# Optimization experiments

Measured on AMD Instinct MI355X. Metric: run time of the kernel, lower is better.

The kernel has to match this reference:

```python
import jax, jax.numpy as jnp
import numpy as np
import math

HIDDEN = 1024
NUM_HEADS = 16
NUM_GROUPS = 16  # source einsum/rearrange only shape-checks when groups == heads
HEAD_DIM = HIDDEN // NUM_HEADS


def rope(x, base=10000.0):
    # x: [b, s, d]; applied to the FULL hidden vector before head split, as in source.
    # Source rope_fn has a reshape bug; this is the intended rotate-half RoPE with
    # half_d frequencies 1/base^(i/half_d) (== 1/base^(2i/d)).
    b, s, d = x.shape
    half = d // 2
    x1, x2 = x[..., :half], x[..., half:]
    pos = jnp.arange(s, dtype=x.dtype)[:, None]                          # [s,1]
    inv_freq = 1.0 / (base ** (jnp.arange(half, dtype=x.dtype) / half))  # [half]
    ang = pos * inv_freq[None, :]                                        # [s,half]
    sin = jnp.sin(ang)[None]                                             # [1,s,half]
    cos = jnp.cos(ang)[None]
    return jnp.concatenate([x1 * cos - x2 * sin, x2 * cos + x1 * sin], axis=-1)


def setup_inputs() -> dict:
    key = jax.random.key(0)
    ks = jax.random.split(key, 10)
    scale = 1.0 / math.sqrt(HIDDEN)
    inp = {
        "x": jax.random.normal(ks[0], (2, 2048, HIDDEN), dtype=jnp.float32),
        "attn_mask": jax.random.randint(ks[1], (2, 2048), 0, 2, dtype=jnp.int32),
        "Wq": jax.random.uniform(ks[2], (HIDDEN, HIDDEN), jnp.float32, -scale, scale),
        "bq": jax.random.uniform(ks[3], (HIDDEN,), jnp.float32, -scale, scale),
        "Wk": jax.random.uniform(ks[4], (HIDDEN, HIDDEN), jnp.float32, -scale, scale),
        "bk": jax.random.uniform(ks[5], (HIDDEN,), jnp.float32, -scale, scale),
        "Wv": jax.random.uniform(ks[6], (HIDDEN, HIDDEN), jnp.float32, -scale, scale),
        "bv": jax.random.uniform(ks[7], (HIDDEN,), jnp.float32, -scale, scale),
        "Wo": jax.random.uniform(ks[8], (HIDDEN, HIDDEN), jnp.float32, -scale, scale),
        "bo": jax.random.uniform(ks[9], (HIDDEN,), jnp.float32, -scale, scale),
    }
    return inp


def reference(x, attn_mask, Wq, bq, Wk, bk, Wv, bv, Wo, bo):
    b, s, _ = x.shape
    g = NUM_GROUPS
    subh = NUM_HEADS // g  # = 1 here
    d = HIDDEN // g        # per-group dim (== head dim when g == h)

    q = rope(x @ Wq.T + bq)
    k = rope(x @ Wk.T + bk)
    v = x @ Wv.T + bv

    # q: b s (g subh d) -> b g subh s d ; k,v: b s (g d) -> b g s d
    q = q.reshape(b, s, g, subh, d).transpose(0, 2, 3, 1, 4)
    k = k.reshape(b, s, g, d).transpose(0, 2, 1, 3)
    v = v.reshape(b, s, g, d).transpose(0, 2, 1, 3)

    e = jnp.einsum('bghqd,bgkd->bghqk', q, k) / math.sqrt(HEAD_DIM)  # [b,g,subh,s,s]
    mask5 = attn_mask[:, None, None, None, :]  # broadcast over g, subh, query
    e = jnp.where(mask5 == 0, -jnp.inf, e)
    attn = jax.nn.softmax(e, axis=-1)
    out = jnp.einsum('bghqk,bgkd->bghqd', attn, v)            # [b,g,subh,s,d]
    out = out.transpose(0, 3, 1, 2, 4).reshape(b, s, HIDDEN)  # b s (g subh d)
    return out @ Wo.T + bo
```

## Files before the change

kernel.cpp:

```cpp
#include <hip/hip_runtime.h>
#include <hip/hip_bf16.h>


constexpr int Bb  = 2;
constexpr int Ss  = 2048;
constexpr int Hh  = 1024;
constexpr int NHh = 16;
constexpr int Mm  = Bb * Ss;

typedef __attribute__((ext_vector_type(8))) unsigned short ushort8;
typedef __attribute__((ext_vector_type(8))) short short8;
typedef __attribute__((ext_vector_type(4))) float f32x4;
typedef __attribute__((ext_vector_type(4))) unsigned int u32x4;

__device__ __forceinline__ unsigned short f2bf(float f) {
    unsigned int u = __float_as_uint(f);
    u += 0x7fffu + ((u >> 16) & 1u);
    return (unsigned short)(u >> 16);
}
__device__ __forceinline__ float bf2f(unsigned short h) {
    return __uint_as_float(((unsigned int)h) << 16);
}
__device__ __forceinline__ void gload16(const void* g, void* l) {
    __builtin_amdgcn_global_load_lds(
        (const __attribute__((address_space(1))) unsigned int*)g,
        (__attribute__((address_space(3))) unsigned int*)l, 16, 0, 0);
}

__global__ __launch_bounds__(256) void convert_k(
    const float* __restrict__ x,
    const float* __restrict__ Wq, const float* __restrict__ Wk,
    const float* __restrict__ Wv, const float* __restrict__ Wo,
    unsigned short* __restrict__ xb, unsigned short* __restrict__ wall)
{
    size_t e = ((size_t)blockIdx.x * 256 + threadIdx.x) << 3;
    const float* s; unsigned short* d;
    if (e < (size_t)Mm * Hh) {
        s = x + e; d = xb + e;
    } else {
        size_t f = e - (size_t)Mm * Hh;
        int t = (int)(f >> 20);
        const float* w = (t == 0) ? Wq : (t == 1) ? Wk : (t == 2) ? Wv : Wo;
        s = w + (f & 1048575);
        d = wall + f;
    }
    float4 a = *(const float4*)s;
    float4 b = *(const float4*)(s + 4);
    ushort8 o;
    o[0] = f2bf(a.x); o[1] = f2bf(a.y); o[2] = f2bf(a.z); o[3] = f2bf(a.w);
    o[4] = f2bf(b.x); o[5] = f2bf(b.y); o[6] = f2bf(b.z); o[7] = f2bf(b.w);
    *(ushort8*)d = o;
}

__global__ __launch_bounds__(256) void maskbf_k(
    const int* __restrict__ am, unsigned short* __restrict__ maskbf)
{
    int i = blockIdx.x * 256 + threadIdx.x;
    maskbf[i] = am[i] ? (unsigned short)0x3F80 : (unsigned short)0;
}

#define GEMM_BODY(ATYPE_PTR, WPTR, K0MAX)                                          \
    __shared__ unsigned short As[128 * 64];                                        \
    __shared__ unsigned short Bs[128 * 64];                                        \
    const int tid  = threadIdx.x;                                                  \
    const int lane = tid & 63;                                                     \
    const int w    = tid >> 6;                                                     \
    const int wr   = w >> 1, wc = w & 1;                                           \
    const int l16  = lane & 15, g = lane >> 4;                                     \
    const int R0   = blockIdx.x * 128;                                             \
    char* asb = (char*)As; char* bsb = (char*)Bs;                                  \
    f32x4 acc[4][4] = {};                                                          \
    for (int k0 = 0; k0 < K0MAX; k0 += 64) {                                       \
        _Pragma("unroll")                                                          \
        for (int it = 0; it < 4; ++it) {                                           \
            int sbase = w * 4096 + it * 1024;                                      \
            int boff  = sbase + lane * 16;                                         \
            int r     = boff >> 7;                                                 \
            int c     = (boff >> 4) & 7;                                           \
            int col   = k0 + ((c ^ (r & 7)) << 3);                                 \
            gload16(&ATYPE_PTR[(size_t)(R0 + r) * 1024 + col], asb + sbase);       \
            gload16(&WPTR[(size_t)(gn + r) * 1024 + col], bsb + sbase);            \
        }                                                                          \
        __syncthreads();                                                           \
        short8 bfrag[4][2];                                                        \
        _Pragma("unroll")                                                          \
        for (int u = 0; u < 4; ++u) {                                              \
            int row = wc * 64 + u * 16 + l16;                                      \
            _Pragma("unroll")                                                      \
            for (int s = 0; s < 2; ++s)                                            \
                bfrag[u][s] = *(const short8*)(bsb + row * 128 +                   \
                               ((s * 64 + g * 16) ^ ((row & 7) << 4)));            \
        }                                                                          \
        _Pragma("unroll")                                                          \
        for (int t = 0; t < 4; ++t) {                                              \
            int row = wr * 64 + t * 16 + l16;                                      \
            short8 af[2];                                                          \
            _Pragma("unroll")                                                      \
            for (int s = 0; s < 2; ++s)                                            \
                af[s] = *(const short8*)(asb + row * 128 +                         \
                         ((s * 64 + g * 16) ^ ((row & 7) << 4)));                  \
            _Pragma("unroll")                                                      \
            for (int u = 0; u < 4; ++u) {                                          \
                acc[t][u] = __builtin_amdgcn_mfma_f32_16x16x32_bf16(af[0], bfrag[u][0], acc[t][u], 0, 0, 0); \
                acc[t][u] = __builtin_amdgcn_mfma_f32_16x16x32_bf16(af[1], bfrag[u][1], acc[t][u], 0, 0, 0); \
            }                                                                      \
        }                                                                          \
        __syncthreads();                                                           \
    }

__global__ __launch_bounds__(256) void gemm_qkv_k(
    const unsigned short* __restrict__ xb, const unsigned short* __restrict__ wall,
    const float* __restrict__ bq, const float* __restrict__ bk, const float* __restrict__ bv,
    unsigned short* __restrict__ q, unsigned short* __restrict__ k2,
    unsigned short* __restrict__ v)
{
    const int gn = blockIdx.y * 128;
    GEMM_BODY(xb, wall, 1024)

    const int sel = gn >> 10;
    const int n0  = gn & 1023;
    const float* bias = (sel == 0) ? bq : (sel == 1) ? bk : bv;
    unsigned short* outp = (sel == 0) ? q : (sel == 1) ? k2 : v;
    const float qs = (sel == 0) ? 0.18033688011112042f : 1.0f;
    #pragma unroll
    for (int u = 0; u < 4; ++u) {
        int coll = wc * 64 + u * 16 + l16;
        float bb = bias[n0 + coll];
        #pragma unroll
        for (int t = 0; t < 4; ++t)
            #pragma unroll
            for (int rr = 0; rr < 4; ++rr) {
                int row = R0 + wr * 64 + t * 16 + g * 4 + rr;
                outp[(size_t)row * 1024 + n0 + coll] = f2bf((acc[t][u][rr] + bb) * qs);
            }
    }
}

__global__ __launch_bounds__(256) void gemm_out_k(
    const unsigned short* __restrict__ ao, const unsigned short* __restrict__ wo,
    const float* __restrict__ bo, float* __restrict__ out)
{
    const int gn = blockIdx.y * 128;
    GEMM_BODY(ao, wo, 1024)

    #pragma unroll
    for (int u = 0; u < 4; ++u) {
        int coll = wc * 64 + u * 16 + l16;
        float bb = bo[gn + coll];
        #pragma unroll
        for (int t = 0; t < 4; ++t)
            #pragma unroll
            for (int rr = 0; rr < 4; ++rr) {
                int row = R0 + wr * 64 + t * 16 + g * 4 + rr;
                out[(size_t)row * 1024 + gn + coll] = acc[t][u][rr] + bb;
            }
    }
}

__global__ __launch_bounds__(256) void rope_frag_k(
    const unsigned short* __restrict__ qin, const unsigned short* __restrict__ kin,
    unsigned short* __restrict__ qfrag, unsigned short* __restrict__ kfrag)
{
    __shared__ unsigned short Ld[2][64][72];
    const int kt = blockIdx.x;
    const int hp = blockIdx.y;
    const int zz = blockIdx.z;
    const int bz = zz & 1, sel = zz >> 1;
    const unsigned short* src = sel ? kin : qin;
    unsigned short* dstf = sel ? kfrag : qfrag;

    const int t   = threadIdx.x;
    const int r   = t & 63;
    const int c16 = (t >> 6) << 4;
    const int pos = kt * 64 + r;
    const size_t rowb = (size_t)(bz * Ss + pos) * 1024;

    ushort8 A0 = *(const ushort8*)&src[rowb + hp * 64 + c16];
    ushort8 A1 = *(const ushort8*)&src[rowb + hp * 64 + c16 + 8];
    ushort8 B0 = *(const ushort8*)&src[rowb + (hp + 8) * 64 + c16];
    ushort8 B1 = *(const ushort8*)&src[rowb + (hp + 8) * 64 + c16 + 8];

    #pragma unroll
    for (int i = 0; i < 16; ++i) {
        int d = c16 + i;
        float jj  = (float)(hp * 64 + d);
        float inv = exp2f(jj * -0.0259525632621414f);
        float ang = (float)pos * inv;
        float sn, cs;
        __sincosf(ang, &sn, &cs);
        unsigned short ua = (i < 8) ? A0[i] : A1[i - 8];
        unsigned short ub = (i < 8) ? B0[i] : B1[i - 8];
        float a = bf2f(ua), b = bf2f(ub);
        Ld[0][r][d] = f2bf(a * cs - b * sn);
        Ld[1][r][d] = f2bf(b * cs + a * sn);
    }
    __syncthreads();

    #pragma unroll
    for (int cc = 0; cc < 4; ++cc) {
        int c    = t * 4 + cc;
        int hh   = c >> 9;
        int ci   = c & 511;
        int blk  = ci >> 7, s2 = (ci >> 6) & 1, lane2 = ci & 63;
        int gg = lane2 >> 4, ll = lane2 & 15;
        ushort8 o = *(const ushort8*)&Ld[hh][blk * 16 + ll][s2 * 32 + gg * 8];
        size_t base = (size_t)(bz * 16 + hp + hh * 8) * 131072 + (size_t)kt * 4096;
        *(ushort8*)&dstf[base + (size_t)ci * 8] = o;
    }
}

__global__ __launch_bounds__(256) void fragify_v_k(
    const unsigned short* __restrict__ v, const int* __restrict__ mask,
    unsigned short* __restrict__ vfrag)
{
    __shared__ unsigned short Ld[64][72];
    __shared__ int Lm[64];
    const int kt = blockIdx.x, bh = blockIdx.y;
    const int bz = bh >> 4, h = bh & 15;
    const int t = threadIdx.x;
    const int r = t & 63, c0 = (t >> 6) << 4;
    const unsigned short* srcp = &v[(size_t)(bz * Ss + kt * 64 + r) * 1024 + h * 64 + c0];
    *(ushort8*)&Ld[r][c0]     = *(const ushort8*)srcp;
    *(ushort8*)&Ld[r][c0 + 8] = *(const ushort8*)(srcp + 8);
    if (t < 64) Lm[t] = mask[bz * Ss + kt * 64 + t];
    __syncthreads();

    #pragma unroll
    for (int cc = 0; cc < 2; ++cc) {
        int c = t * 2 + cc;
        int dt4 = c >> 7, ks = (c >> 6) & 1, lane2 = c & 63;
        int gg = lane2 >> 4, ll = lane2 & 15;
        ushort8 o;
        #pragma unroll
        for (int e = 0; e < 8; ++e) {
            int key = ks * 32 + gg * 8 + e;
            o[e] = Lm[key] ? Ld[key][dt4 * 16 + ll] : (unsigned short)0;
        }
        *(ushort8*)&vfrag[(size_t)bh * 131072 + (size_t)kt * 4096 + (size_t)c * 8] = o;
    }
}

__global__ __launch_bounds__(256, 3) void flash_k(
    const unsigned short* __restrict__ qfrag, const unsigned short* __restrict__ kfrag,
    const unsigned short* __restrict__ vfrag, const unsigned short* __restrict__ maskbf,
    unsigned short* __restrict__ opart, float2* __restrict__ ml)
{
    const int F   = blockIdx.x;
    const int xcd = F & 7, j = F >> 3;
    const int grp = xcd * 4 + (j >> 5);
    const int rem = j & 31;
    const int qb  = rem >> 1;
    const int half = rem & 1;
    const int h   = grp & 15;
    const int bz  = grp >> 4;
    const int kt0 = half * 16;

    const int tid  = threadIdx.x;
    const int lane = tid & 63;
    const int w    = tid >> 6;
    const int l16  = lane & 15;
    const int g    = lane >> 4;

    const size_t fb = (size_t)(bz * 16 + h) * 131072;
    const unsigned short* kfb = kfrag + fb;
    const unsigned short* vfb = vfrag + fb;
    const unsigned short* qfb = qfrag + fb;

    const unsigned short* kp = kfb + (size_t)kt0 * 4096 + lane * 8;
    const unsigned short* vp = vfb + (size_t)kt0 * 4096 + lane * 8;
    const unsigned short* mp = maskbf + bz * Ss + kt0 * 64 + g * 8;

    short8 qf[2][2];
    #pragma unroll
    for (int t = 0; t < 2; ++t)
        #pragma unroll
        for (int s = 0; s < 2; ++s)
            qf[t][s] = *(const short8*)&qfb[(size_t)(qb * 8 + w * 2 + t) * 1024
                                            + s * 512 + lane * 8];

    f32x4 O[2][4];
    #pragma unroll
    for (int t = 0; t < 2; ++t)
        #pragma unroll
        for (int d = 0; d < 4; ++d) O[t][d] = (f32x4)0.f;
    f32x4 Osum[2];
    Osum[0] = (f32x4)0.f; Osum[1] = (f32x4)0.f;
    float mrow[2] = {-1.0e4f, -1.0e4f};
    const f32x4 Zf = (f32x4)0.f;

    for (int it = 0; it < 16; ++it) {
        short8 KC[8];
        #pragma unroll
        for (int i = 0; i < 4; ++i) KC[i]     = *(const short8*)(kp + i * 512);
        #pragma unroll
        for (int i = 0; i < 4; ++i) KC[4 + i] = *(const short8*)(kp + 2048 + i * 512);
        short8 mf[2];
        mf[0] = *(const short8*)mp;
        mf[1] = *(const short8*)(mp + 32);

        f32x4 S[2][4];
        #pragma unroll
        for (int k4 = 0; k4 < 4; ++k4)
            #pragma unroll
            for (int t = 0; t < 2; ++t) {
                S[t][k4] = __builtin_amdgcn_mfma_f32_16x16x32_bf16(
                    KC[k4 * 2 + 0], qf[t][0], Zf, 0, 0, 0);
                S[t][k4] = __builtin_amdgcn_mfma_f32_16x16x32_bf16(
                    KC[k4 * 2 + 1], qf[t][1], S[t][k4], 0, 0, 0);
            }

        short8 V0[4];
        #pragma unroll
        for (int dt = 0; dt < 4; ++dt)
            V0[dt] = *(const short8*)(vp + dt * 1024);

        float rm[2];
        #pragma unroll
        for (int t = 0; t < 2; ++t) {
            float m0 = fmaxf(fmaxf(S[t][0][0], S[t][0][1]), fmaxf(S[t][0][2], S[t][0][3]));
            float m1 = fmaxf(fmaxf(S[t][1][0], S[t][1][1]), fmaxf(S[t][1][2], S[t][1][3]));
            float m2 = fmaxf(fmaxf(S[t][2][0], S[t][2][1]), fmaxf(S[t][2][2], S[t][2][3]));
            float m3 = fmaxf(fmaxf(S[t][3][0], S[t][3][1]), fmaxf(S[t][3][2], S[t][3][3]));
            float m  = fmaxf(fmaxf(m0, m1), fmaxf(m2, m3));
            m = fmaxf(m, __shfl_xor(m, 16));
            m = fmaxf(m, __shfl_xor(m, 32));
            rm[t] = m;
        }

        bool grow = (rm[0] > mrow[0] + 10.0f) || (rm[1] > mrow[1] + 10.0f);
        if (__any((int)grow)) {
            float mn0 = fmaxf(mrow[0], rm[0]);
            float mn1 = fmaxf(mrow[1], rm[1]);
            float rs0 = exp2f(mrow[0] - mn0);
            float rs1 = exp2f(mrow[1] - mn1);
            mrow[0] = mn0; mrow[1] = mn1;
            #pragma unroll
            for (int r = 0; r < 4; ++r) {
                float f0 = __shfl(rs0, g * 4 + r);
                float f1 = __shfl(rs1, g * 4 + r);
                #pragma unroll
                for (int dt = 0; dt < 4; ++dt) { O[0][dt][r] *= f0; O[1][dt][r] *= f1; }
                Osum[0][r] *= f0; Osum[1][r] *= f1;
            }
        }

        short8 V1[4];
        #pragma unroll
        for (int dt = 0; dt < 4; ++dt)
            V1[dt] = *(const short8*)(vp + 512 + dt * 1024);

        #pragma unroll
        for (int t = 0; t < 2; ++t) {
            unsigned int U[4][2];
            #pragma unroll
            for (int k4 = 0; k4 < 4; ++k4) {
                float p0 = exp2f(S[t][k4][0] - mrow[t]);
                float p1 = exp2f(S[t][k4][1] - mrow[t]);
                float p2 = exp2f(S[t][k4][2] - mrow[t]);
                float p3 = exp2f(S[t][k4][3] - mrow[t]);
                asm("v_cvt_pk_bf16_f32 %0, %1, %2" : "=v"(U[k4][0]) : "v"(p0), "v"(p1));
                asm("v_cvt_pk_bf16_f32 %0, %1, %2" : "=v"(U[k4][1]) : "v"(p2), "v"(p3));
            }
            asm("v_permlane32_swap_b32 %0, %1" : "+v"(U[0][0]), "+v"(U[1][0]));
            asm("v_permlane32_swap_b32 %0, %1" : "+v"(U[0][1]), "+v"(U[1][1]));
            asm("v_permlane32_swap_b32 %0, %1" : "+v"(U[2][0]), "+v"(U[3][0]));
            asm("v_permlane32_swap_b32 %0, %1" : "+v"(U[2][1]), "+v"(U[3][1]));
            asm("v_permlane16_swap_b32 %0, %1" : "+v"(U[0][0]), "+v"(U[1][0]));
            asm("v_permlane16_swap_b32 %0, %1" : "+v"(U[0][1]), "+v"(U[1][1]));
            asm("v_permlane16_swap_b32 %0, %1" : "+v"(U[2][0]), "+v"(U[3][0]));
            asm("v_permlane16_swap_b32 %0, %1" : "+v"(U[2][1]), "+v"(U[3][1]));

            u32x4 gp0, gp1;
            gp0[0] = U[0][0]; gp0[1] = U[0][1]; gp0[2] = U[1][0]; gp0[3] = U[1][1];
            gp1[0] = U[2][0]; gp1[1] = U[2][1]; gp1[2] = U[3][0]; gp1[3] = U[3][1];
            short8 pf0 = __builtin_bit_cast(short8, gp0);
            short8 pf1 = __builtin_bit_cast(short8, gp1);

            Osum[t] = __builtin_amdgcn_mfma_f32_16x16x32_bf16(pf0, mf[0], Osum[t], 0, 0, 0);
            #pragma unroll
            for (int dt = 0; dt < 4; ++dt)
                O[t][dt] = __builtin_amdgcn_mfma_f32_16x16x32_bf16(pf0, V0[dt], O[t][dt], 0, 0, 0);
            Osum[t] = __builtin_amdgcn_mfma_f32_16x16x32_bf16(pf1, mf[1], Osum[t], 0, 0, 0);
            #pragma unroll
            for (int dt = 0; dt < 4; ++dt)
                O[t][dt] = __builtin_amdgcn_mfma_f32_16x16x32_bf16(pf1, V1[dt], O[t][dt], 0, 0, 0);
        }

        kp += 4096; vp += 4096; mp += 64;
    }

    const size_t NE = (size_t)Mm * Hh;
    #pragma unroll
    for (int t = 0; t < 2; ++t)
        #pragma unroll
        for (int r = 0; r < 4; ++r) {
            float osum = Osum[t][r];
            float inv  = osum > 0.f ? 1.0f / osum : 0.f;
            float mo   = __shfl(mrow[t], g * 4 + r);
            int rowl   = qb * 128 + w * 32 + t * 16 + g * 4 + r;
            size_t ob  = (size_t)half * NE
                       + ((size_t)(bz * Ss + rowl)) * 1024 + h * 64;
            #pragma unroll
            for (int dt = 0; dt < 4; ++dt)
                opart[ob + dt * 16 + l16] = f2bf(O[t][dt][r] * inv);
            if (l16 == 0)
                ml[((half * 2 + bz) * 16 + h) * 2048 + rowl] = make_float2(mo, osum);
        }
}

__global__ __launch_bounds__(256) void combine_k(
    const unsigned short* __restrict__ opart, const float2* __restrict__ ml,
    unsigned short* __restrict__ ao)
{
    const size_t NE = (size_t)Mm * Hh;
    int c    = blockIdx.x * 256 + threadIdx.x;
    int row  = c >> 7;
    int col8 = c & 127;
    int h    = col8 >> 3;
    int bz   = row >> 11, qrow = row & 2047;

    float2 a = ml[((0 * 2 + bz) * 16 + h) * 2048 + qrow];
    float2 b = ml[((1 * 2 + bz) * 16 + h) * 2048 + qrow];
    float M  = fmaxf(a.x, b.x);
    float w1 = exp2f(a.x - M) * a.y;
    float w2 = exp2f(b.x - M) * b.y;
    float tot = w1 + w2;
    float inv = tot > 0.f ? 1.0f / tot : 0.f;
    w1 *= inv; w2 *= inv;

    ushort8 o1 = *(const ushort8*)&opart[(size_t)c * 8];
    ushort8 o2 = *(const ushort8*)&opart[NE + (size_t)c * 8];
    ushort8 o;
    #pragma unroll
    for (int jj = 0; jj < 8; ++jj)
        o[jj] = f2bf(bf2f(o1[jj]) * w1 + bf2f(o2[jj]) * w2);
    *(ushort8*)&ao[(size_t)c * 8] = o;
}

extern "C" void kernel_launch(void* const* d_in, const int* in_sizes, int n_in,
                              void* d_out, int out_size, void* d_ws, size_t ws_size,
                              hipStream_t stream)
{
    const float* x  = (const float*)d_in[0];
    const int*   am = (const int*)d_in[1];
    const float* Wq = (const float*)d_in[2];
    const float* bq = (const float*)d_in[3];
    const float* Wk = (const float*)d_in[4];
    const float* bk = (const float*)d_in[5];
    const float* Wv = (const float*)d_in[6];
    const float* bv = (const float*)d_in[7];
    const float* Wo = (const float*)d_in[8];
    const float* bo = (const float*)d_in[9];
    float* out = (float*)d_out;

    const size_t NE = (size_t)Mm * Hh;
    unsigned short* q     = (unsigned short*)d_ws;
    unsigned short* k     = q + NE;
    unsigned short* v     = k + NE;
    unsigned short* ao    = v + NE;
    unsigned short* xb    = ao + NE;
    unsigned short* wall  = xb + NE;
    unsigned short* wo    = wall + 3u * 1048576u;
    unsigned short* kfrag = wall + 4u * 1048576u;
    unsigned short* qfrag = xb;
    unsigned short* vfrag = q;
    unsigned short* opart = k;
    float2*         ml    = (float2*)(kfrag + 4u * 1048576u);
    unsigned short* maskbf = (unsigned short*)(ml + 131072);

    convert_k<<<(2 * NE) / (256 * 8), 256, 0, stream>>>(x, Wq, Wk, Wv, Wo, xb, wall);
    maskbf_k<<<dim3(Mm / 256), 256, 0, stream>>>(am, maskbf);
    gemm_qkv_k<<<dim3(Mm / 128, 3072 / 128), 256, 0, stream>>>(
        xb, wall, bq, bk, bv, q, k, v);
    rope_frag_k<<<dim3(32, 8, 4), 256, 0, stream>>>(q, k, qfrag, kfrag);
    fragify_v_k<<<dim3(32, 32), 256, 0, stream>>>(v, am, vfrag);
    flash_k<<<dim3(1024), 256, 0, stream>>>(qfrag, kfrag, vfrag, maskbf, opart, ml);
    combine_k<<<dim3((Mm * 128) / 256), 256, 0, stream>>>(opart, ml, ao);
    gemm_out_k<<<dim3(Mm / 128, Hh / 128), 256, 0, stream>>>(ao, wo, bo, out);
}
```

Baseline: 164.9 us.

## Stage K/V tiles through double-buffered LDS with async global-to-LDS prefetch

The flash attention kernel now cooperatively loads each 64-key K and V tile into a double-buffered LDS array with global_load_lds, prefetching the next tile while computing on the current one. Previously every wave read the same K/V fragments directly from global memory. This cuts redundant global and L2 traffic across the 4 waves and overlaps loads with MFMA work. In exchange it uses 32KB of LDS per block, which may limit occupancy under launch_bounds(256,3), and adds a __syncthreads per iteration.

New measurement: 167.6 us. About the same (+1.6%).

```diff
diff --git a/kernel.cpp b/kernel.cpp
--- a/kernel.cpp
+++ b/kernel.cpp
@@ -245,6 +245,9 @@
     const unsigned short* __restrict__ vfrag, const unsigned short* __restrict__ maskbf,
     unsigned short* __restrict__ opart, float2* __restrict__ ml)
 {
+    __shared__ unsigned short Ks[2][4096];
+    __shared__ unsigned short Vs[2][4096];
+
     const int F   = blockIdx.x;
     const int xcd = F & 7, j = F >> 3;
     const int grp = xcd * 4 + (j >> 5);
@@ -262,13 +265,12 @@
     const int g    = lane >> 4;
 
     const size_t fb = (size_t)(bz * 16 + h) * 131072;
-    const unsigned short* kfb = kfrag + fb;
-    const unsigned short* vfb = vfrag + fb;
+    const unsigned short* kp  = kfrag + fb + (size_t)kt0 * 4096;
+    const unsigned short* vp  = vfrag + fb + (size_t)kt0 * 4096;
+    const unsigned short* mp  = maskbf + bz * Ss + kt0 * 64 + g * 8;
     const unsigned short* qfb = qfrag + fb;
 
-    const unsigned short* kp = kfb + (size_t)kt0 * 4096 + lane * 8;
-    const unsigned short* vp = vfb + (size_t)kt0 * 4096 + lane * 8;
-    const unsigned short* mp = maskbf + bz * Ss + kt0 * 64 + g * 8;
+    const int so = w * 512 + lane * 8;
 
     short8 qf[2][2];
     #pragma unroll
@@ -288,15 +290,35 @@
     float mrow[2] = {-1.0e4f, -1.0e4f};
     const f32x4 Zf = (f32x4)0.f;
 
+    gload16(kp + so,        (char*)&Ks[0][w * 512]);
+    gload16(kp + 2048 + so, (char*)&Ks[0][2048 + w * 512]);
+    gload16(vp + so,        (char*)&Vs[0][w * 512]);
+    gload16(vp + 2048 + so, (char*)&Vs[0][2048 + w * 512]);
+    __syncthreads();
+
     for (int it = 0; it < 16; ++it) {
+        const int cur = it & 1;
+
+        if (it + 1 < 16) {
+            const unsigned short* kn = kp + (size_t)(it + 1) * 4096;
+            const unsigned short* vn = vp + (size_t)(it + 1) * 4096;
+            gload16(kn + so,        (char*)&Ks[cur ^ 1][w * 512]);
+            gload16(kn + 2048 + so, (char*)&Ks[cur ^ 1][2048 + w * 512]);
+            gload16(vn + so,        (char*)&Vs[cur ^ 1][w * 512]);
+            gload16(vn + 2048 + so, (char*)&Vs[cur ^ 1][2048 + w * 512]);
+        }
+
+        const unsigned short* ksb = &Ks[cur][0];
+        const unsigned short* vsb = &Vs[cur][0];
+        const unsigned short* mpi = mp + it * 64;
+
         short8 KC[8];
         #pragma unroll
-        for (int i = 0; i < 4; ++i) KC[i]     = *(const short8*)(kp + i * 512);
-        #pragma unroll
-        for (int i = 0; i < 4; ++i) KC[4 + i] = *(const short8*)(kp + 2048 + i * 512);
+        for (int i = 0; i < 8; ++i)
+            KC[i] = *(const short8*)&ksb[i * 512 + lane * 8];
         short8 mf[2];
-        mf[0] = *(const short8*)mp;
-        mf[1] = *(const short8*)(mp + 32);
+        mf[0] = *(const short8*)mpi;
+        mf[1] = *(const short8*)(mpi + 32);
 
         f32x4 S[2][4];
         #pragma unroll
@@ -312,7 +334,7 @@
         short8 V0[4];
         #pragma unroll
         for (int dt = 0; dt < 4; ++dt)
-            V0[dt] = *(const short8*)(vp + dt * 1024);
+            V0[dt] = *(const short8*)&vsb[dt * 1024 + lane * 8];
 
         float rm[2];
         #pragma unroll
@@ -347,7 +369,7 @@
         short8 V1[4];
         #pragma unroll
         for (int dt = 0; dt < 4; ++dt)
-            V1[dt] = *(const short8*)(vp + 512 + dt * 1024);
+            V1[dt] = *(const short8*)&vsb[512 + dt * 1024 + lane * 8];
 
         #pragma unroll
         for (int t = 0; t < 2; ++t) {
@@ -386,7 +408,7 @@
                 O[t][dt] = __builtin_amdgcn_mfma_f32_16x16x32_bf16(pf1, V1[dt], O[t][dt], 0, 0, 0);
         }
 
-        kp += 4096; vp += 4096; mp += 64;
+        __syncthreads();
     }
 
     const size_t NE = (size_t)Mm * Hh;
```
